# Performance work log

Measured on AMD Instinct MI355X. Metric: run time of the kernel, lower is better.

Reference implementation:

```python
import jax, jax.numpy as jnp
import numpy as np
from jax import lax

N, T, D, W, H, V = 256, 64, 1280, 256, 512, 10000
NULL_IDX = 0  # ignore_index


def setup_inputs() -> dict:
    key = jax.random.key(0)
    ks = jax.random.split(key, 9)
    features = jax.random.normal(ks[0], (N, D), dtype=jnp.float32)
    captions = jax.random.randint(ks[1], (N, T + 1), 0, V, dtype=jnp.int64)
    # learned parameters
    W_proj = jax.random.normal(ks[2], (D, H), dtype=jnp.float32) / np.sqrt(D)
    b_proj = jnp.zeros((H,), dtype=jnp.float32)
    W_embed = jax.random.normal(ks[3], (V, W), dtype=jnp.float32) / np.sqrt(V)
    Wx = jax.random.normal(ks[4], (W, H), dtype=jnp.float32) / np.sqrt(W)
    Wh = jax.random.normal(ks[5], (H, H), dtype=jnp.float32) / np.sqrt(H)
    b = jnp.zeros((H,), dtype=jnp.float32)
    W_out = jax.random.normal(ks[6], (H, V), dtype=jnp.float32) / np.sqrt(H)
    b_out = jnp.zeros((V,), dtype=jnp.float32)
    return {"features": features, "captions": captions, "W_proj": W_proj,
            "b_proj": b_proj, "W_embed": W_embed, "Wx": Wx, "Wh": Wh, "b": b,
            "W_out": W_out, "b_out": b_out}


def reference(features, captions, W_proj, b_proj, W_embed, Wx, Wh, b, W_out, b_out):
    captions_in = captions[:, :-1]   # (N, T)
    captions_out = captions[:, 1:]   # (N, T)

    h0 = features @ W_proj + b_proj                      # (N, H)
    x = W_embed[captions_in]                             # (N, T, W)
    # Precompute input-to-hidden part; recurrence only needs h @ Wh.
    xWxb = jnp.einsum('ntw,wh->nth', x, Wx) + b          # (N, T, H)

    def step(h_prev, xt):
        h_next = jnp.tanh(h_prev @ Wh + xt)
        return h_next, h_next

    _, hs = lax.scan(step, h0, jnp.swapaxes(xWxb, 0, 1))  # (T, N, H)
    h = jnp.swapaxes(hs, 0, 1)                            # (N, T, H)

    scores = jnp.einsum('nth,hv->ntv', h, W_out) + b_out  # (N, T, V)
    logp = jax.nn.log_softmax(scores, axis=-1)
    nll = -jnp.take_along_axis(logp, captions_out[..., None], axis=-1)[..., 0]
    mask = (captions_out != NULL_IDX).astype(nll.dtype)
    loss = jnp.sum(nll * mask) / N
    return loss
```

## Files before the change

kernel.cpp:

```cpp
#include <hip/hip_runtime.h>
#include <hip/hip_bf16.h>
#include <hip/hip_fp8.h>

#define NB 256
#define TT 64
#define DD 1280
#define WW 256
#define HH 512
#define VV 10000
#define VP 10112
#define NCT 79
#define MROWS (NB*TT)

typedef short short8 __attribute__((ext_vector_type(8)));
typedef float f32x4 __attribute__((ext_vector_type(4)));
typedef int   int4v __attribute__((ext_vector_type(4)));
typedef int   int8v __attribute__((ext_vector_type(8)));

static __device__ __forceinline__ unsigned short f2bf(float x){
    unsigned int u = __float_as_uint(x);
    unsigned int r = u + 0x7FFFu + ((u >> 16) & 1u);
    return (unsigned short)(r >> 16);
}
static __device__ __forceinline__ float bf2f(unsigned short u){
    return __uint_as_float(((unsigned int)u) << 16);
}
static __device__ __forceinline__ unsigned char f2f8(float x){
    __hip_fp8_e4m3 q(x);
    return (unsigned char)q.__x;
}
static __device__ __forceinline__ float f82f(unsigned char b){
    __hip_fp8_e4m3 q; q.__x = b;
    return (float)q;
}
static __device__ __forceinline__ unsigned enc4(float x){
    unsigned s = (x < 0.f) ? 8u : 0u;
    float a = fabsf(x);
    unsigned m;
    if      (a < 0.25f) m = 0;
    else if (a < 0.75f) m = 1;
    else if (a < 1.25f) m = 2;
    else if (a < 1.75f) m = 3;
    else if (a < 2.5f)  m = 4;
    else if (a < 3.5f)  m = 5;
    else if (a < 5.0f)  m = 6;
    else                m = 7;
    return s | m;
}
static __device__ __forceinline__ void gload16b(const unsigned char* g, unsigned char* l){
    __builtin_amdgcn_global_load_lds(
        (const __attribute__((address_space(1))) void*)g,
        (__attribute__((address_space(3))) void*)l, 16, 0, 0);
}


__global__ __launch_bounds__(256) void k_prep(const float* __restrict__ W_proj,
                                              unsigned short* __restrict__ Wpb,
                                              const float* __restrict__ Wx,
                                              unsigned short* __restrict__ WxT,
                                              const float* __restrict__ Wh,
                                              unsigned char* __restrict__ WhT4,
                                              const float* __restrict__ W_out,
                                              unsigned char* __restrict__ WoT8p,
                                              const float* __restrict__ bo,
                                              float* __restrict__ bop){
    __shared__ unsigned short tileS[64][17];
    int b = blockIdx.x;
    int tid = threadIdx.x;
    if (b < 640){
        int i = b*256 + tid;
        float4 f = *reinterpret_cast<const float4*>(W_proj + (size_t)i*4);
        unsigned short* o = Wpb + (size_t)i*4;
        o[0]=f2bf(f.x); o[1]=f2bf(f.y); o[2]=f2bf(f.z); o[3]=f2bf(f.w);
    } else if (b < 768){
        int r = b - 640;
        int c0 = (r & 7)*64, r0 = (r >> 3)*16;
        int c = tid & 63, rr = tid >> 6;
        #pragma unroll
        for (int j = 0; j < 4; ++j){
            int rw_ = rr + j*4;
            tileS[c][rw_] = f2bf(Wx[(size_t)(r0+rw_)*HH + c0 + c]);
        }
        __syncthreads();
        int rw = tid & 15, cw = tid >> 4;
        #pragma unroll
        for (int j = 0; j < 4; ++j){
            int c2 = cw + j*16;
            WxT[(size_t)(c0+c2)*WW + r0 + rw] = tileS[c2][rw];
        }
    } else if (b < 1280){
        int r = b - 768;
        int j = r >> 1;
        int col = (r & 1)*256 + tid;
        float w0 = Wh[(size_t)(2*j  )*HH + col] * 32.0f;
        float w1 = Wh[(size_t)(2*j+1)*HH + col] * 32.0f;
        WhT4[(size_t)col*256 + j] = (unsigned char)(enc4(w0) | (enc4(w1) << 4));
    } else if (b < 6336){
        unsigned char (*tileC)[20] = reinterpret_cast<unsigned char (*)[20]>(&tileS[0][0]);
        int r = b - 1280;
        int c0 = (r % 158)*64, r0 = (r / 158)*16;
        int c = tid & 63, rr = tid >> 6;
        #pragma unroll
        for (int j = 0; j < 4; ++j){
            int rw_ = rr + j*4;
            unsigned char v = 0;
            if (c0 + c < VV) v = f2f8(W_out[(size_t)(r0+rw_)*VV + c0 + c]);
            tileC[c][rw_] = v;
        }
        __syncthreads();
        int rw = tid & 15, cw = tid >> 4;
        #pragma unroll
        for (int j = 0; j < 4; ++j){
            int c2 = cw + j*16;
            int col = c0 + c2, k = r0 + rw;
            if (col < VP){
                size_t addr = ((size_t)((col >> 7)*4 + (k >> 7)))*16384
                            + (unsigned)((col & 127)*128 + (k & 127));
                WoT8p[addr] = tileC[c2][rw];
            }
        }
    } else {
        int i = (b - 6336)*256 + tid;
        if (i < VP) bop[i] = (i < VV) ? bo[i]*1.44269504f : -30000.0f;
    }
}

__global__ __launch_bounds__(512) void k_h0(const float* __restrict__ feat,
                                            const unsigned short* __restrict__ Wpb,
                                            const float* __restrict__ bp,
                                            float* __restrict__ h0){
    int n0 = blockIdx.x*2;
    int h = threadIdx.x;
    const float* f0 = feat + (size_t)(n0+0)*DD;
    const float* f1 = feat + (size_t)(n0+1)*DD;
    float a0=0.f, a1=0.f;
    for (int d = 0; d < DD; d += 4){
        #pragma unroll
        for (int j = 0; j < 4; ++j){
            float w = bf2f(Wpb[(size_t)(d+j)*HH + h]);
            a0 += f0[d+j]*w;
            a1 += f1[d+j]*w;
        }
    }
    float bb = bp[h];
    h0[(size_t)(n0+0)*HH+h] = a0+bb;
    h0[(size_t)(n0+1)*HH+h] = a1+bb;
}

__global__ __launch_bounds__(256) void k_e2(const float* __restrict__ We,
                                            const unsigned short* __restrict__ WxT,
                                            const float* __restrict__ bias,
                                            unsigned short* __restrict__ E2b){
    int lane = threadIdx.x & 63;
    int wv   = threadIdx.x >> 6;
    int l15 = lane & 15, lhi = lane >> 4;
    int rbase = blockIdx.x*64 + wv*16;
    int arow = rbase + l15; if (arow > VV-1) arow = VV-1;
    short8 a[8];
    #pragma unroll
    for (int kk = 0; kk < 8; ++kk){
        const float* src = We + (size_t)arow*WW + kk*32 + lhi*8;
        float4 g0 = *reinterpret_cast<const float4*>(src);
        float4 g1 = *reinterpret_cast<const float4*>(src + 4);
        short8 v;
        v[0]=(short)f2bf(g0.x); v[1]=(short)f2bf(g0.y); v[2]=(short)f2bf(g0.z); v[3]=(short)f2bf(g0.w);
        v[4]=(short)f2bf(g1.x); v[5]=(short)f2bf(g1.y); v[6]=(short)f2bf(g1.z); v[7]=(short)f2bf(g1.w);
        a[kk] = v;
    }
    int ct0 = blockIdx.y*16;
    for (int ct = ct0; ct < ct0+16; ++ct){
        int c0 = ct*16;
        f32x4 acc = {0.f,0.f,0.f,0.f};
        #pragma unroll
        for (int kk = 0; kk < 8; ++kk){
            short8 b = *reinterpret_cast<const short8*>(WxT + (size_t)(c0 + l15)*WW + kk*32 + lhi*8);
            acc = __builtin_amdgcn_mfma_f32_16x16x32_bf16(a[kk], b, acc, 0, 0, 0);
        }
        float bb = bias[c0 + l15];
        #pragma unroll
        for (int r = 0; r < 4; ++r){
            int row = rbase + lhi*4 + r;
            if (row < VV) E2b[(size_t)row*HH + c0 + l15] = f2bf(acc[r] + bb);
        }
    }
}

__global__ __launch_bounds__(512, 2) void k_rnn(const float* __restrict__ h0,
                                                const unsigned char* __restrict__ WhT4,
                                                const unsigned short* __restrict__ E2b,
                                                const int* __restrict__ caps,
                                                unsigned char* __restrict__ hA8){
    __shared__ __align__(32) unsigned char hl[2][HH];
    int tid = threadIdx.x;
    int lane = tid & 63, wv = tid >> 6;
    int l15 = lane & 15, lhi = lane >> 4;
    int n = blockIdx.x;
    int c0w = wv*64;
    int mycol = c0w + lane;
    unsigned char* hbase = hA8 + ((size_t)((n>>1)*4 + (wv>>1)))*16384
                               + (unsigned)((n&1)*64*128 + (mycol & 127));

    int4v b[4][4];
    #pragma unroll
    for (int ct = 0; ct < 4; ++ct){
        int col = c0w + ct*16 + l15;
        #pragma unroll
        for (int kt = 0; kt < 4; ++kt){
            b[ct][kt] = *reinterpret_cast<const int4v*>(WhT4 + (size_t)col*256 + kt*64 + lhi*16);
            asm volatile("" : "+v"(b[ct][kt]));
        }
    }
    hl[0][tid] = f2f8(h0[(size_t)n*HH + tid]);
    __syncthreads();
    int cur = 0;
    for (int t = 0; t < TT; ++t){
        int tok = caps[n*(TT+1) + t];
        unsigned short xv = E2b[(size_t)tok*HH + mycol];
        int8v a[4];
        #pragma unroll
        for (int kt = 0; kt < 4; ++kt)
            a[kt] = *reinterpret_cast<const int8v*>(&hl[cur][kt*128 + lhi*32]);
        f32x4 acc[4];
        #pragma unroll
        for (int ct = 0; ct < 4; ++ct){
            acc[ct] = (f32x4){0.f,0.f,0.f,0.f};
            #pragma unroll
            for (int kt = 0; kt < 4; ++kt){
                int8v bb = __builtin_shufflevector(b[ct][kt], b[ct][kt], 0,1,2,3,0,1,2,3);
                acc[ct] = __builtin_amdgcn_mfma_scale_f32_16x16x128_f8f6f4(
                    a[kt], bb, acc[ct],
                    0, 4,
                    0, (int)0x7F7F7F7F,
                    0, (int)0x7A7A7A7A);
            }
        }
        float v = (lhi == 0) ? acc[0][0] : (lhi == 1) ? acc[1][0]
                : (lhi == 2) ? acc[2][0] : acc[3][0];
        float x = v + bf2f(xv);
        float e = __expf(2.f*x);
        float th = 1.f - 2.f/(e + 1.f);
        unsigned char hv = f2f8(th);
        hl[cur^1][mycol] = hv;
        hbase[t*128] = hv;
        __syncthreads();
        cur ^= 1;
    }
}

__global__ __launch_bounds__(512) void k_scores(const unsigned char* __restrict__ hA8,
                                                const unsigned char* __restrict__ WoT8p,
                                                const float* __restrict__ bop,
                                                float* __restrict__ pps){
    __shared__ unsigned char As[16384];
    __shared__ unsigned char Bs[16384];
    int bid = blockIdx.x;
    int x = bid & 7;
    int local = bid >> 3;
    int ct = local >> 4;
    int rt = x*16 + (local & 15);

    int tid = threadIdx.x;
    int lane = tid & 63, wv = tid >> 6;
    int l15 = lane & 15, lhi = lane >> 4;
    int wr = wv >> 1, wc = wv & 1;
    const unsigned char* Abase = hA8   + (size_t)rt*65536;
    const unsigned char* Bbase = WoT8p + (size_t)ct*65536;

    unsigned coff[2];
    #pragma unroll
    for (int i = 0; i < 2; ++i){
        unsigned chunk = (unsigned)(i*512 + tid);
        unsigned rowloc = chunk >> 3;
        coff[i] = rowloc*128 + (((chunk & 7u) ^ (rowloc & 7u))*16u);
    }

    f32x4 acc[2][4];
    #pragma unroll
    for (int m = 0; m < 2; ++m)
        #pragma unroll
        for (int n = 0; n < 4; ++n)
            acc[m][n] = (f32x4){0.f,0.f,0.f,0.f};

    for (int kt = 0; kt < 4; ++kt){
        #pragma unroll
        for (int i = 0; i < 2; ++i){
            gload16b(Abase + kt*16384 + coff[i], As + (unsigned)((i*512 + tid) * 16));
            gload16b(Bbase + kt*16384 + coff[i], Bs + (unsigned)((i*512 + tid) * 16));
        }
        __syncthreads();
        int8v af[2];
        #pragma unroll
        for (int m = 0; m < 2; ++m){
            unsigned row = (unsigned)(wr*32 + m*16 + l15);
            int4v c0 = *reinterpret_cast<const int4v*>(As + row*128 + (((unsigned)(lhi*2+0) ^ (row&7))*16));
            int4v c1 = *reinterpret_cast<const int4v*>(As + row*128 + (((unsigned)(lhi*2+1) ^ (row&7))*16));
            af[m] = __builtin_shufflevector(c0, c1, 0,1,2,3,4,5,6,7);
        }
        #pragma unroll
        for (int n = 0; n < 4; ++n){
            unsigned col = (unsigned)(wc*64 + n*16 + l15);
            int4v c0 = *reinterpret_cast<const int4v*>(Bs + col*128 + (((unsigned)(lhi*2+0) ^ (col&7))*16));
            int4v c1 = *reinterpret_cast<const int4v*>(Bs + col*128 + (((unsigned)(lhi*2+1) ^ (col&7))*16));
            int8v bf = __builtin_shufflevector(c0, c1, 0,1,2,3,4,5,6,7);
            #pragma unroll
            for (int m = 0; m < 2; ++m)
                acc[m][n] = __builtin_amdgcn_mfma_scale_f32_16x16x128_f8f6f4(
                    af[m], bf, acc[m][n],
                    0, 0,
                    0, (int)0x7F7F7F7F,
                    0, (int)0x7F7F7F7F);
        }
        __syncthreads();
    }

    const float LOG2E = 1.44269504f;
    float srun[2][4];
    #pragma unroll
    for (int m = 0; m < 2; ++m)
        #pragma unroll
        for (int r = 0; r < 4; ++r) srun[m][r] = 0.f;
    #pragma unroll
    for (int n = 0; n < 4; ++n){
        int colg = ct*128 + wc*64 + n*16 + l15;
        float bb2 = bop[colg];
        #pragma unroll
        for (int m = 0; m < 2; ++m)
            #pragma unroll
            for (int r = 0; r < 4; ++r)
                srun[m][r] += exp2f(fmaf(acc[m][n][r], LOG2E, bb2));
    }
    #pragma unroll
    for (int off = 1; off < 16; off <<= 1)
        #pragma unroll
        for (int m = 0; m < 2; ++m)
            #pragma unroll
            for (int r = 0; r < 4; ++r)
                srun[m][r] += __shfl_xor(srun[m][r], off, 64);
    float* red = (float*)As;
    if (wc == 1 && l15 == 0){
        #pragma unroll
        for (int m = 0; m < 2; ++m)
            #pragma unroll
            for (int r = 0; r < 4; ++r){
                int ri = wr*32 + m*16 + lhi*4 + r;
                red[ri] = srun[m][r];
            }
    }
    __syncthreads();
    if (wc == 0 && l15 == 0){
        #pragma unroll
        for (int m = 0; m < 2; ++m)
            #pragma unroll
            for (int r = 0; r < 4; ++r){
                int ri = wr*32 + m*16 + lhi*4 + r;
                int gr = rt*128 + ri;
                pps[(size_t)ct*MROWS + gr] = srun[m][r] + red[ri];
            }
    }
}

__global__ __launch_bounds__(256) void k_tsc(const unsigned char* __restrict__ hA8,
                                             const unsigned char* __restrict__ WoT8p,
                                             const float* __restrict__ bo,
                                             const int* __restrict__ caps,
                                             float* __restrict__ t0arr){
    int lane = threadIdx.x & 63, w = threadIdx.x >> 6;
    int row = blockIdx.x*4 + w;
    int tgt = caps[(row >> 6)*(TT+1) + (row & 63) + 1];
    int k0 = lane*8;
    int ktile = k0 >> 7, kin = k0 & 127;
    const unsigned char* hp = hA8   + ((size_t)((row >> 7)*4 + ktile))*16384
                                    + (unsigned)((row & 127)*128 + kin);
    const unsigned char* wp = WoT8p + ((size_t)((tgt >> 7)*4 + ktile))*16384
                                    + (unsigned)((tgt & 127)*128 + kin);
    float sum = 0.f;
    #pragma unroll
    for (int j = 0; j < 8; ++j)
        sum += f82f(hp[j]) * f82f(wp[j]);
    #pragma unroll
    for (int off = 1; off < 64; off <<= 1)
        sum += __shfl_xor(sum, off, 64);
    if (lane == 0) t0arr[row] = sum + bo[tgt];
}

__global__ __launch_bounds__(256) void k_loss1(const float* __restrict__ pps,
                                               const float* __restrict__ t0arr,
                                               const int* __restrict__ caps,
                                               float* __restrict__ bsum){
    __shared__ float reds[256];
    int tid = threadIdx.x;
    int rloc = tid & 63, q = tid >> 6;
    int row = blockIdx.x*64 + rloc;
    int c0 = q*20, c1 = (q == 3) ? NCT : c0 + 20;
    float s = 0.f;
    for (int ct = c0; ct < c1; ++ct)
        s += pps[(size_t)ct*MROWS + row];
    reds[tid] = s;
    __syncthreads();
    if (q == 0){
        s = reds[rloc] + reds[64+rloc] + reds[128+rloc] + reds[192+rloc];
        int tgt = caps[(row >> 6)*(TT+1) + (row & 63) + 1];
        reds[rloc] = (tgt != 0) ? (__logf(s) - t0arr[row]) : 0.f;
    }
    __syncthreads();
    if (tid < 32) reds[tid] += reds[tid+32];
    __syncthreads();
    if (tid < 16) reds[tid] += reds[tid+16];
    __syncthreads();
    if (tid < 8)  reds[tid] += reds[tid+8];
    __syncthreads();
    if (tid < 4)  reds[tid] += reds[tid+4];
    __syncthreads();
    if (tid == 0) bsum[blockIdx.x] = reds[0] + reds[1] + reds[2] + reds[3];
}

__global__ __launch_bounds__(64) void k_loss2(const float* __restrict__ bsum, float* __restrict__ out){
    __shared__ float red[64];
    int tid = threadIdx.x;
    red[tid] = bsum[tid] + bsum[tid+64] + bsum[tid+128] + bsum[tid+192];
    __syncthreads();
    for (int off = 32; off > 0; off >>= 1){
        if (tid < off) red[tid] += red[tid+off];
        __syncthreads();
    }
    if (tid == 0) out[0] = red[0] / (float)NB;
}

extern "C" void kernel_launch(void* const* d_in, const int* in_sizes, int n_in,
                              void* d_out, int out_size, void* d_ws, size_t ws_size,
                              hipStream_t stream) {
    const float* features = (const float*)d_in[0];
    const int*   captions = (const int*)  d_in[1];
    const float* W_proj   = (const float*)d_in[2];
    const float* b_proj   = (const float*)d_in[3];
    const float* W_embed  = (const float*)d_in[4];
    const float* Wx       = (const float*)d_in[5];
    const float* Wh       = (const float*)d_in[6];
    const float* b_       = (const float*)d_in[7];
    const float* W_out    = (const float*)d_in[8];
    const float* b_out    = (const float*)d_in[9];
    float* out = (float*)d_out;

    char* ws = (char*)d_ws;
    unsigned short* E2b   = (unsigned short*)(ws + 0);
    float*          h0    = (float*)         (ws + 10240000);
    unsigned char*  WhT4  = (unsigned char*) (ws + 10764288);
    unsigned short* WxT   = (unsigned short*)(ws + 10895360);
    unsigned char*  WoT8p = (unsigned char*) (ws + 11157504);
    float*          bop   = (float*)         (ws + 16334848);
    unsigned char*  hA8   = (unsigned char*) (ws + 16375296);
    float*          pps   = (float*)         (ws + 24763904);
    float*          t0arr = (float*)         (ws + 29941248);
    float*          bsum  = (float*)         (ws + 30006784);
    unsigned short* Wpb   = (unsigned short*)(ws + 30007808);
    if (ws_size < 31318528u) return;

    k_prep<<<6376, 256, 0, stream>>>(W_proj, Wpb, Wx, WxT, Wh, WhT4, W_out, WoT8p, b_out, bop);
    k_h0<<<NB/2, 512, 0, stream>>>(features, Wpb, b_proj, h0);
    k_e2<<<dim3(157,2), 256, 0, stream>>>(W_embed, WxT, b_, E2b);
    k_rnn<<<NB, 512, 0, stream>>>(h0, WhT4, E2b, captions, hA8);
    k_scores<<<128*NCT, 512, 0, stream>>>(hA8, WoT8p, bop, pps);
    k_tsc<<<MROWS/4, 256, 0, stream>>>(hA8, WoT8p, b_out, captions, t0arr);
    k_loss1<<<256, 256, 0, stream>>>(pps, t0arr, captions, bsum);
    k_loss2<<<1, 64, 0, stream>>>(bsum, out);
}
```

Before: 302.2 us.

## Fold h0 projection into prep, split E2 grid wider, break RNN MFMA chain

Computes h0 directly from fp32 W_proj inside the prep kernel, which removes the separate bf16 conversion pass and one launch. Doubles the E2 grid's y-dimension so each block handles fewer column tiles. In the recurrent kernel, each MFMA now accumulates into its own zeroed accumulator and the partials are summed afterwards, removing the serial MFMA dependency chain. This raises register pressure, and the launch-bounds occupancy hint is dropped to make room.

```diff
diff --git a/kernel.cpp b/kernel.cpp
--- a/kernel.cpp
+++ b/kernel.cpp
@@ -54,8 +54,10 @@
 }
 
 
-__global__ __launch_bounds__(256) void k_prep(const float* __restrict__ W_proj,
-                                              unsigned short* __restrict__ Wpb,
+__global__ __launch_bounds__(256) void k_prep(const float* __restrict__ feat,
+                                              const float* __restrict__ W_proj,
+                                              const float* __restrict__ bp,
+                                              float* __restrict__ h0,
                                               const float* __restrict__ Wx,
                                               unsigned short* __restrict__ WxT,
                                               const float* __restrict__ Wh,
@@ -65,15 +67,24 @@
                                               const float* __restrict__ bo,
                                               float* __restrict__ bop){
     __shared__ unsigned short tileS[64][17];
+    __shared__ float fs[DD];
     int b = blockIdx.x;
     int tid = threadIdx.x;
-    if (b < 640){
-        int i = b*256 + tid;
-        float4 f = *reinterpret_cast<const float4*>(W_proj + (size_t)i*4);
-        unsigned short* o = Wpb + (size_t)i*4;
-        o[0]=f2bf(f.x); o[1]=f2bf(f.y); o[2]=f2bf(f.z); o[3]=f2bf(f.w);
-    } else if (b < 768){
-        int r = b - 640;
+    if (b < 256){
+        int n = b;
+        for (int i = tid; i < DD; i += 256) fs[i] = feat[(size_t)n*DD + i];
+        __syncthreads();
+        int c0 = tid, c1 = tid + 256;
+        float a0 = 0.f, a1 = 0.f;
+        for (int d = 0; d < DD; ++d){
+            float fv = fs[d];
+            a0 += fv * W_proj[(size_t)d*HH + c0];
+            a1 += fv * W_proj[(size_t)d*HH + c1];
+        }
+        h0[(size_t)n*HH + c0] = a0 + bp[c0];
+        h0[(size_t)n*HH + c1] = a1 + bp[c1];
+    } else if (b < 384){
+        int r = b - 256;
         int c0 = (r & 7)*64, r0 = (r >> 3)*16;
         int c = tid & 63, rr = tid >> 6;
         #pragma unroll
@@ -88,16 +99,16 @@
             int c2 = cw + j*16;
             WxT[(size_t)(c0+c2)*WW + r0 + rw] = tileS[c2][rw];
         }
-    } else if (b < 1280){
-        int r = b - 768;
+    } else if (b < 896){
+        int r = b - 384;
         int j = r >> 1;
         int col = (r & 1)*256 + tid;
         float w0 = Wh[(size_t)(2*j  )*HH + col] * 32.0f;
         float w1 = Wh[(size_t)(2*j+1)*HH + col] * 32.0f;
         WhT4[(size_t)col*256 + j] = (unsigned char)(enc4(w0) | (enc4(w1) << 4));
-    } else if (b < 6336){
+    } else if (b < 5952){
         unsigned char (*tileC)[20] = reinterpret_cast<unsigned char (*)[20]>(&tileS[0][0]);
-        int r = b - 1280;
+        int r = b - 896;
         int c0 = (r % 158)*64, r0 = (r / 158)*16;
         int c = tid & 63, rr = tid >> 6;
         #pragma unroll
@@ -120,31 +131,9 @@
             }
         }
     } else {
-        int i = (b - 6336)*256 + tid;
+        int i = (b - 5952)*256 + tid;
         if (i < VP) bop[i] = (i < VV) ? bo[i]*1.44269504f : -30000.0f;
     }
-}
-
-__global__ __launch_bounds__(512) void k_h0(const float* __restrict__ feat,
-                                            const unsigned short* __restrict__ Wpb,
-                                            const float* __restrict__ bp,
-                                            float* __restrict__ h0){
-    int n0 = blockIdx.x*2;
-    int h = threadIdx.x;
-    const float* f0 = feat + (size_t)(n0+0)*DD;
-    const float* f1 = feat + (size_t)(n0+1)*DD;
-    float a0=0.f, a1=0.f;
-    for (int d = 0; d < DD; d += 4){
-        #pragma unroll
-        for (int j = 0; j < 4; ++j){
-            float w = bf2f(Wpb[(size_t)(d+j)*HH + h]);
-            a0 += f0[d+j]*w;
-            a1 += f1[d+j]*w;
-        }
-    }
-    float bb = bp[h];
-    h0[(size_t)(n0+0)*HH+h] = a0+bb;
-    h0[(size_t)(n0+1)*HH+h] = a1+bb;
 }
 
 __global__ __launch_bounds__(256) void k_e2(const float* __restrict__ We,
@@ -167,8 +156,8 @@
         v[4]=(short)f2bf(g1.x); v[5]=(short)f2bf(g1.y); v[6]=(short)f2bf(g1.z); v[7]=(short)f2bf(g1.w);
         a[kk] = v;
     }
-    int ct0 = blockIdx.y*16;
-    for (int ct = ct0; ct < ct0+16; ++ct){
+    int ct0 = blockIdx.y*8;
+    for (int ct = ct0; ct < ct0+8; ++ct){
         int c0 = ct*16;
         f32x4 acc = {0.f,0.f,0.f,0.f};
         #pragma unroll
@@ -185,11 +174,11 @@
     }
 }
 
-__global__ __launch_bounds__(512, 2) void k_rnn(const float* __restrict__ h0,
-                                                const unsigned char* __restrict__ WhT4,
-                                                const unsigned short* __restrict__ E2b,
-                                                const int* __restrict__ caps,
-                                                unsigned char* __restrict__ hA8){
+__global__ __launch_bounds__(512) void k_rnn(const float* __restrict__ h0,
+                                             const unsigned char* __restrict__ WhT4,
+                                             const unsigned short* __restrict__ E2b,
+                                             const int* __restrict__ caps,
+                                             unsigned char* __restrict__ hA8){
     __shared__ __align__(32) unsigned char hl[2][HH];
     int tid = threadIdx.x;
     int lane = tid & 63, wv = tid >> 6;
@@ -213,6 +202,7 @@
     hl[0][tid] = f2f8(h0[(size_t)n*HH + tid]);
     __syncthreads();
     int cur = 0;
+    const f32x4 z = {0.f,0.f,0.f,0.f};
     for (int t = 0; t < TT; ++t){
         int tok = caps[n*(TT+1) + t];
         unsigned short xv = E2b[(size_t)tok*HH + mycol];
@@ -220,22 +210,23 @@
         #pragma unroll
         for (int kt = 0; kt < 4; ++kt)
             a[kt] = *reinterpret_cast<const int8v*>(&hl[cur][kt*128 + lhi*32]);
-        f32x4 acc[4];
-        #pragma unroll
-        for (int ct = 0; ct < 4; ++ct){
-            acc[ct] = (f32x4){0.f,0.f,0.f,0.f};
+        f32x4 acc[4][4];
+        #pragma unroll
+        for (int ct = 0; ct < 4; ++ct)
             #pragma unroll
             for (int kt = 0; kt < 4; ++kt){
                 int8v bb = __builtin_shufflevector(b[ct][kt], b[ct][kt], 0,1,2,3,0,1,2,3);
-                acc[ct] = __builtin_amdgcn_mfma_scale_f32_16x16x128_f8f6f4(
-                    a[kt], bb, acc[ct],
+                acc[ct][kt] = __builtin_amdgcn_mfma_scale_f32_16x16x128_f8f6f4(
+                    a[kt], bb, z,
                     0, 4,
                     0, (int)0x7F7F7F7F,
                     0, (int)0x7A7A7A7A);
             }
-        }
-        float v = (lhi == 0) ? acc[0][0] : (lhi == 1) ? acc[1][0]
-                : (lhi == 2) ? acc[2][0] : acc[3][0];
+        float s0 = (acc[0][0][0] + acc[0][1][0]) + (acc[0][2][0] + acc[0][3][0]);
+        float s1 = (acc[1][0][0] + acc[1][1][0]) + (acc[1][2][0] + acc[1][3][0]);
+        float s2 = (acc[2][0][0] + acc[2][1][0]) + (acc[2][2][0] + acc[2][3][0]);
+        float s3 = (acc[3][0][0] + acc[3][1][0]) + (acc[3][2][0] + acc[3][3][0]);
+        float v = (lhi == 0) ? s0 : (lhi == 1) ? s1 : (lhi == 2) ? s2 : s3;
         float x = v + bf2f(xv);
         float e = __expf(2.f*x);
         float th = 1.f - 2.f/(e + 1.f);
@@ -452,12 +443,11 @@
     float*          pps   = (float*)         (ws + 24763904);
     float*          t0arr = (float*)         (ws + 29941248);
     float*          bsum  = (float*)         (ws + 30006784);
-    unsigned short* Wpb   = (unsigned short*)(ws + 30007808);
-    if (ws_size < 31318528u) return;
-
-    k_prep<<<6376, 256, 0, stream>>>(W_proj, Wpb, Wx, WxT, Wh, WhT4, W_out, WoT8p, b_out, bop);
-    k_h0<<<NB/2, 512, 0, stream>>>(features, Wpb, b_proj, h0);
-    k_e2<<<dim3(157,2), 256, 0, stream>>>(W_embed, WxT, b_, E2b);
+    if (ws_size < 30007808u) return;
+
+    k_prep<<<5992, 256, 0, stream>>>(features, W_proj, b_proj, h0,
+                                     Wx, WxT, Wh, WhT4, W_out, WoT8p, b_out, bop);
+    k_e2<<<dim3(157,4), 256, 0, stream>>>(W_embed, WxT, b_, E2b);
     k_rnn<<<NB, 512, 0, stream>>>(h0, WhT4, E2b, captions, hA8);
     k_scores<<<128*NCT, 512, 0, stream>>>(hA8, WoT8p, bop, pps);
     k_tsc<<<MROWS/4, 256, 0, stream>>>(hA8, WoT8p, b_out, captions, t0arr);
```

After: 295.0 us, median of 2. 1.02x faster.
